# Performance work log

Measured on AMD Instinct MI355X. Metric: run time of the kernel, lower is better.

Reference implementation:

```python
import jax, jax.numpy as jnp
import numpy as np

B, N_IN, N_OUT = 4, 1024, 1024
IN_CH_RAW, OUT_CH = 7, 16
IN_CH = IN_CH_RAW + 1  # density channel appended
INIT_LENGTH_SCALE = 0.1


def setup_inputs() -> dict:
    key = jax.random.key(0)
    k1, k2, k3, k4 = jax.random.split(key, 4)
    context_x = jax.random.normal(k1, (B, N_IN, 1), dtype=jnp.float32)
    context_y = jax.random.normal(k2, (B, N_IN, IN_CH_RAW), dtype=jnp.float32)
    t = jax.random.normal(k3, (B, N_OUT, 1), dtype=jnp.float32)
    sigma = jnp.full((IN_CH,), np.log(INIT_LENGTH_SCALE), dtype=jnp.float32)
    W = jax.random.normal(k4, (IN_CH, OUT_CH), dtype=jnp.float32) * 0.05
    b = jnp.zeros((OUT_CH,), dtype=jnp.float32)
    return {"context_x": context_x, "context_y": context_y, "t": t,
            "sigma": sigma, "W": W, "b": b}


def reference(context_x, context_y, t, sigma, W, b):
    # context_x: (B, n_in, 1), t: (B, n_out, 1)
    # squared pairwise distances (1-D inputs): (B, n_in, n_out)
    d2 = jnp.square(context_x[:, :, None, 0] - t[:, None, :, 0])
    scales = jnp.exp(sigma)  # (C,) per-channel length scales
    # RBF weights: (B, n_in, n_out, C)
    wt = jnp.exp(-0.5 * d2[..., None] / jnp.square(scales))
    # append density channel: (B, n_in, C)
    density = jnp.ones(context_y.shape[:2] + (1,), dtype=context_y.dtype)
    y = jnp.concatenate([density, context_y], axis=2)
    # weighted sum over context points: (B, n_out, C)
    agg = jnp.einsum('bic,bioc->boc', y, wt)
    den, conv = agg[..., :1], agg[..., 1:]
    agg = jnp.concatenate([den, conv / (den + 1e-8)], axis=-1)
    # final linear: (B, n_out, out_channels)
    return agg @ W + b
```

## Files before the change

kernel.cpp:

```cpp
#include <hip/hip_runtime.h>

#define NB 4
#define N_IN 1024
#define N_OUT 1024
#define IN_CH_RAW 7
#define CH 8
#define OUT_CH 16
#define LOG2E 1.4426950408889634f

__device__ __forceinline__ float wave_sum(float x) {
    float s = x;
    int v;
    v = __builtin_amdgcn_update_dpp(0, __float_as_int(s), 0x111, 0xF, 0xF, true); s += __int_as_float(v);
    v = __builtin_amdgcn_update_dpp(0, __float_as_int(s), 0x112, 0xF, 0xF, true); s += __int_as_float(v);
    v = __builtin_amdgcn_update_dpp(0, __float_as_int(s), 0x114, 0xF, 0xF, true); s += __int_as_float(v);
    v = __builtin_amdgcn_update_dpp(0, __float_as_int(s), 0x118, 0xF, 0xF, true); s += __int_as_float(v);
    v = __builtin_amdgcn_update_dpp(0, __float_as_int(s), 0x142, 0xF, 0xF, true); s += __int_as_float(v);
    v = __builtin_amdgcn_update_dpp(0, __float_as_int(s), 0x143, 0xF, 0xF, true); s += __int_as_float(v);
    return __int_as_float(__builtin_amdgcn_readlane(__float_as_int(s), 63));
}

__global__ __launch_bounds__(256) void convdeepset_kernel(
    const float* __restrict__ cx,
    const float* __restrict__ cy,
    const float* __restrict__ t,
    const float* __restrict__ sigma,
    const float* __restrict__ W,
    const float* __restrict__ bias,
    float* __restrict__ out)
{
    __shared__ float4 lds4[N_IN * 2];

    const int tid = threadIdx.x;
    const int bi  = blockIdx.x;
    const int b   = bi >> 7;

    #pragma unroll
    for (int k = 0; k < 4; ++k) {
        const int r = tid + 256 * k;
        const float x = cx[b * N_IN + r];
        const float* yr = cy + ((size_t)(b * N_IN + r)) * IN_CH_RAW;
        const float4 q0 = make_float4(x,     yr[0], yr[1], yr[2]);
        const float4 q1 = make_float4(yr[3], yr[4], yr[5], yr[6]);
        const int idx = (r * 2) ^ ((r & 4) >> 2);
        lds4[idx]     = q0;
        lds4[idx ^ 1] = q1;
    }

    const float s0 = sigma[0];
    bool uni = true;
    float kc2[CH];
    #pragma unroll
    for (int c = 0; c < CH; ++c) {
        const float sc = sigma[c];
        kc2[c] = -0.5f * LOG2E * __expf(-2.0f * sc);
        uni = uni && (sc == s0);
    }
    const float ks = __expf(-s0) * sqrtf(0.5f * LOG2E);

    const int wave = tid >> 6;
    const int lane = tid & 63;
    const int p0   = bi * 8 + wave * 2;
    const int o0   = p0 & (N_OUT - 1);
    const float t0 = t[b * N_OUT + o0];
    const float t1 = t[b * N_OUT + o0 + 1];
    const float ntk0 = -(t0 * ks);
    const float ntk1 = -(t1 * ks);

    const int slot0 = (lane * 2) ^ ((lane & 4) >> 2);
    const int slot1 = slot0 ^ 1;

    float a0[CH], a1[CH];
    #pragma unroll
    for (int c = 0; c < CH; ++c) { a0[c] = 0.0f; a1[c] = 0.0f; }

    __syncthreads();

    if (uni) {
        #pragma unroll
        for (int k = 0; k < 16; ++k) {
            const float4 q0 = lds4[slot0 + 128 * k];
            const float4 q1 = lds4[slot1 + 128 * k];
            const float d0 = __fmaf_rn(q0.x, ks, ntk0);
            const float d1 = __fmaf_rn(q0.x, ks, ntk1);
            const float w0 = exp2f(-(d0 * d0));
            const float w1 = exp2f(-(d1 * d1));
            a0[0] += w0;        a1[0] += w1;
            a0[1] += w0 * q0.y; a1[1] += w1 * q0.y;
            a0[2] += w0 * q0.z; a1[2] += w1 * q0.z;
            a0[3] += w0 * q0.w; a1[3] += w1 * q0.w;
            a0[4] += w0 * q1.x; a1[4] += w1 * q1.x;
            a0[5] += w0 * q1.y; a1[5] += w1 * q1.y;
            a0[6] += w0 * q1.z; a1[6] += w1 * q1.z;
            a0[7] += w0 * q1.w; a1[7] += w1 * q1.w;
        }
    } else {
        #pragma unroll 2
        for (int k = 0; k < 16; ++k) {
            const float4 q0 = lds4[slot0 + 128 * k];
            const float4 q1 = lds4[slot1 + 128 * k];
            const float y[IN_CH_RAW] = {q0.y, q0.z, q0.w, q1.x, q1.y, q1.z, q1.w};
            const float dx0 = q0.x - t0, d20 = dx0 * dx0;
            const float dx1 = q0.x - t1, d21 = dx1 * dx1;
            a0[0] += exp2f(d20 * kc2[0]);
            a1[0] += exp2f(d21 * kc2[0]);
            #pragma unroll
            for (int c = 1; c < CH; ++c) {
                a0[c] += exp2f(d20 * kc2[c]) * y[c - 1];
                a1[c] += exp2f(d21 * kc2[c]) * y[c - 1];
            }
        }
    }

    float r0[CH], r1[CH];
    #pragma unroll
    for (int c = 0; c < CH; ++c) { r0[c] = wave_sum(a0[c]); r1[c] = wave_sum(a1[c]); }

    if (lane < 32) {
        const int sel = lane >> 4;
        const int col = lane & 15;
        float a[CH];
        #pragma unroll
        for (int c = 0; c < CH; ++c) a[c] = sel ? r1[c] : r0[c];
        const float inv = 1.0f / (a[0] + 1e-8f);
        float v = bias[col] + a[0] * W[col];
        #pragma unroll
        for (int c = 1; c < CH; ++c) v += (a[c] * inv) * W[c * OUT_CH + col];
        out[(size_t)(p0 + sel) * OUT_CH + col] = v;
    }
}

extern "C" void kernel_launch(void* const* d_in, const int* in_sizes, int n_in,
                              void* d_out, int out_size, void* d_ws, size_t ws_size,
                              hipStream_t stream) {
    const float* cx    = (const float*)d_in[0];
    const float* cy    = (const float*)d_in[1];
    const float* t     = (const float*)d_in[2];
    const float* sigma = (const float*)d_in[3];
    const float* W     = (const float*)d_in[4];
    const float* bias  = (const float*)d_in[5];
    float* out = (float*)d_out;

    dim3 grid(NB * N_OUT / 8), block(256);
    convdeepset_kernel<<<grid, block, 0, stream>>>(cx, cy, t, sigma, W, bias, out);
}
```

Before: 9.983 us.

## Vectorize context staging loads and pack dual-output accumulators into float2

The LDS staging now has each thread load four consecutive context points with seven float4 loads of context_y and one float4 of context_x, replacing strided scalar loads. The swizzle index changes to match the new point-to-thread mapping. The uniform-sigma inner loop keeps its two per-output accumulators as float2 vectors so the compiler can emit packed FP32 FMA/mul instructions (v_pk_fma_f32 on CDNA3-class hardware). This aims to cut load instruction count and VALU issue slots, at the cost of more registers held during staging.

```diff
diff --git a/kernel.cpp b/kernel.cpp
--- a/kernel.cpp
+++ b/kernel.cpp
@@ -7,6 +7,8 @@
 #define CH 8
 #define OUT_CH 16
 #define LOG2E 1.4426950408889634f
+
+typedef float v2f __attribute__((ext_vector_type(2)));
 
 __device__ __forceinline__ float wave_sum(float x) {
     float s = x;
@@ -35,16 +37,22 @@
     const int bi  = blockIdx.x;
     const int b   = bi >> 7;
 
-    #pragma unroll
-    for (int k = 0; k < 4; ++k) {
-        const int r = tid + 256 * k;
-        const float x = cx[b * N_IN + r];
-        const float* yr = cy + ((size_t)(b * N_IN + r)) * IN_CH_RAW;
-        const float4 q0 = make_float4(x,     yr[0], yr[1], yr[2]);
-        const float4 q1 = make_float4(yr[3], yr[4], yr[5], yr[6]);
-        const int idx = (r * 2) ^ ((r & 4) >> 2);
-        lds4[idx]     = q0;
-        lds4[idx ^ 1] = q1;
+    {
+        const float4* cyv = reinterpret_cast<const float4*>(
+            cy + (size_t)b * N_IN * IN_CH_RAW + tid * 28);
+        float4 f[7];
+        #pragma unroll
+        for (int k = 0; k < 7; ++k) f[k] = cyv[k];
+        const float4 xv = *reinterpret_cast<const float4*>(cx + b * N_IN + 4 * tid);
+        const float xarr[4] = {xv.x, xv.y, xv.z, xv.w};
+        const float* yf = reinterpret_cast<const float*>(f);
+        #pragma unroll
+        for (int j = 0; j < 4; ++j) {
+            const float* yr = yf + 7 * j;
+            const int idx = (8 * tid + 2 * j) ^ (tid & 1);
+            lds4[idx]     = make_float4(xarr[j], yr[0], yr[1], yr[2]);
+            lds4[idx ^ 1] = make_float4(yr[3], yr[4], yr[5], yr[6]);
+        }
     }
 
     const float s0 = sigma[0];
@@ -64,15 +72,15 @@
     const int o0   = p0 & (N_OUT - 1);
     const float t0 = t[b * N_OUT + o0];
     const float t1 = t[b * N_OUT + o0 + 1];
-    const float ntk0 = -(t0 * ks);
-    const float ntk1 = -(t1 * ks);
+    const v2f ks2  = {ks, ks};
+    const v2f ntk  = {-(t0 * ks), -(t1 * ks)};
 
     const int slot0 = (lane * 2) ^ ((lane & 4) >> 2);
     const int slot1 = slot0 ^ 1;
 
-    float a0[CH], a1[CH];
+    v2f acc2[CH];
     #pragma unroll
-    for (int c = 0; c < CH; ++c) { a0[c] = 0.0f; a1[c] = 0.0f; }
+    for (int c = 0; c < CH; ++c) acc2[c] = (v2f){0.0f, 0.0f};
 
     __syncthreads();
 
@@ -81,18 +89,18 @@
         for (int k = 0; k < 16; ++k) {
             const float4 q0 = lds4[slot0 + 128 * k];
             const float4 q1 = lds4[slot1 + 128 * k];
-            const float d0 = __fmaf_rn(q0.x, ks, ntk0);
-            const float d1 = __fmaf_rn(q0.x, ks, ntk1);
-            const float w0 = exp2f(-(d0 * d0));
-            const float w1 = exp2f(-(d1 * d1));
-            a0[0] += w0;        a1[0] += w1;
-            a0[1] += w0 * q0.y; a1[1] += w1 * q0.y;
-            a0[2] += w0 * q0.z; a1[2] += w1 * q0.z;
-            a0[3] += w0 * q0.w; a1[3] += w1 * q0.w;
-            a0[4] += w0 * q1.x; a1[4] += w1 * q1.x;
-            a0[5] += w0 * q1.y; a1[5] += w1 * q1.y;
-            a0[6] += w0 * q1.z; a1[6] += w1 * q1.z;
-            a0[7] += w0 * q1.w; a1[7] += w1 * q1.w;
+            const v2f xx = {q0.x, q0.x};
+            const v2f d  = xx * ks2 + ntk;
+            const v2f nd2 = -(d * d);
+            const v2f w  = {exp2f(nd2.x), exp2f(nd2.y)};
+            acc2[0] += w;
+            acc2[1] += w * q0.y;
+            acc2[2] += w * q0.z;
+            acc2[3] += w * q0.w;
+            acc2[4] += w * q1.x;
+            acc2[5] += w * q1.y;
+            acc2[6] += w * q1.z;
+            acc2[7] += w * q1.w;
         }
     } else {
         #pragma unroll 2
@@ -102,19 +110,20 @@
             const float y[IN_CH_RAW] = {q0.y, q0.z, q0.w, q1.x, q1.y, q1.z, q1.w};
             const float dx0 = q0.x - t0, d20 = dx0 * dx0;
             const float dx1 = q0.x - t1, d21 = dx1 * dx1;
-            a0[0] += exp2f(d20 * kc2[0]);
-            a1[0] += exp2f(d21 * kc2[0]);
+            acc2[0] += (v2f){exp2f(d20 * kc2[0]), exp2f(d21 * kc2[0])};
             #pragma unroll
-            for (int c = 1; c < CH; ++c) {
-                a0[c] += exp2f(d20 * kc2[c]) * y[c - 1];
-                a1[c] += exp2f(d21 * kc2[c]) * y[c - 1];
-            }
+            for (int c = 1; c < CH; ++c)
+                acc2[c] += (v2f){exp2f(d20 * kc2[c]) * y[c - 1],
+                                 exp2f(d21 * kc2[c]) * y[c - 1]};
         }
     }
 
     float r0[CH], r1[CH];
     #pragma unroll
-    for (int c = 0; c < CH; ++c) { r0[c] = wave_sum(a0[c]); r1[c] = wave_sum(a1[c]); }
+    for (int c = 0; c < CH; ++c) {
+        r0[c] = wave_sum(acc2[c].x);
+        r1[c] = wave_sum(acc2[c].y);
+    }
 
     if (lane < 32) {
         const int sel = lane >> 4;
```

Measured after the change: 10.07 us. About the same (+0.9%).
